# Kernel optimization log

Measured on AMD Instinct MI355X. Metric: run time of the kernel, lower is better.

## Reference

```python
import jax, jax.numpy as jnp
import numpy as np

N, D, E, K, L, NF, VOCAB = 100000, 128, 600000, 3, 3, 9, 100
BN_EPS = 1e-5
S = 0.05


def setup_inputs() -> dict:
    key = jax.random.key(0)
    ks = jax.random.split(key, 8)
    return {
        "x": jax.random.randint(ks[0], (N, NF), 0, VOCAB),
        "k_edges": jax.random.randint(ks[1], (K, 2, E), 0, N),
        "emb_tables": jax.random.normal(ks[2], (NF, VOCAB, D), jnp.float32) * S,
        "W1": jax.random.normal(ks[3], (L, D, 2 * D), jnp.float32) * S,
        "b1": jnp.zeros((L, 2 * D), jnp.float32),
        "g1": jnp.ones((L, 2 * D), jnp.float32),
        "be1": jnp.zeros((L, 2 * D), jnp.float32),
        "W2": jax.random.normal(ks[4], (L, 2 * D, D), jnp.float32) * S,
        "b2": jnp.zeros((L, D), jnp.float32),
        "eps": jnp.zeros((L,), jnp.float32),
        "alpha": jnp.zeros((L, K), jnp.float32),
        "bn_g": jnp.ones((L, D), jnp.float32),
        "bn_b": jnp.zeros((L, D), jnp.float32),
    }


def _bn(h, g, b):
    # training-mode BatchNorm1d over the node (batch) axis
    mu = h.mean(axis=0)
    var = h.var(axis=0)
    return (h - mu) * jax.lax.rsqrt(var + BN_EPS) * g + b


def _gin(h, src, dst, eps_l, W1_l, b1_l, g1_l, be1_l, W2_l, b2_l):
    # NodeGINConv (train_eps): mlp((1+eps)*x + sum_{j->i} x_j)
    agg = jax.ops.segment_sum(h[src], dst, num_segments=N)  # [N, D]
    z = (1.0 + eps_l) * h + agg
    z = jax.nn.relu(_bn(z @ W1_l + b1_l, g1_l, be1_l))  # [N, 2D]
    return z @ W2_l + b2_l  # [N, D]


def reference(x, k_edges, emb_tables, W1, b1, g1, be1, W2, b2, eps, alpha, bn_g, bn_b):
    # AtomEncoder: sum of per-feature embedding lookups -> [N, D]
    h = jnp.take_along_axis(
        emb_tables.transpose(1, 0, 2),  # [VOCAB, NF, D]
        x.T[..., None].transpose(1, 0, 2) * 0 + 0,  # placeholder avoided below
        axis=0,
    ) if False else emb_tables[jnp.arange(NF)[None, :], x].sum(axis=1)
    for l in range(L):
        # one shared wrapped GIN conv applied to each of the K relational edge sets
        msgs = jax.vmap(
            lambda e: _gin(h, e[0], e[1], eps[l], W1[l], b1[l], g1[l], be1[l], W2[l], b2[l])
        )(k_edges)  # [K, N, D]
        a = jax.nn.softmax(alpha[l])  # [K]
        h = jnp.einsum('knd,k->nd', msgs, a)
        h = jax.nn.relu(_bn(h, bn_g[l], bn_b[l]))  # dropout p=0 / eval -> identity
    return h
```

## Files before the change

### kernel.cpp

```cpp
#include <hip/hip_runtime.h>

#define NV     100000
#define DD     128
#define D2     256
#define EE     600000
#define KK     3
#define LL     3
#define NFEAT  9
#define VOCABS 100

#define NBKT   196
#define BCAP   8192

typedef __attribute__((ext_vector_type(8))) short short8;
typedef __attribute__((ext_vector_type(4))) float f32x4;
typedef __attribute__((ext_vector_type(2))) float f32x2;
typedef __attribute__((ext_vector_type(4))) unsigned int uint4v;

#define PA      0
#define PA2     8
#define PB2     136
#define PA1K(k) (264 + (k)*512)
#define PB1K(k) (264 + (k)*512 + 256)

#define ZS(k)  ((k)*512)
#define ZQ(k)  ((k)*512 + 256)
#define HSUM   1536
#define HSQ    1664

#define HB_OFF   ((size_t)0)
#define ZIN_OFF  ((size_t)25700000)
#define HNB_OFF  ((size_t)102500000)
#define O_BASE   ((size_t)128100000)

__device__ __forceinline__ unsigned short f2bf(float f) {
    union { float f; unsigned int u; } v; v.f = f;
    return (unsigned short)((v.u + 0x7FFFu + ((v.u >> 16) & 1u)) >> 16);
}
__device__ __forceinline__ float bf2f(unsigned short u) {
    union { unsigned int u; float f; } v; v.u = ((unsigned int)u) << 16;
    return v.f;
}
__device__ __forceinline__ f32x2 up2(unsigned int v) {
    union { unsigned int u[2]; f32x2 f; } w;
    w.u[0] = v << 16;
    w.u[1] = v & 0xFFFF0000u;
    return w.f;
}

__global__ void k_embed(const int* __restrict__ x, const float* __restrict__ emb,
                        unsigned short* __restrict__ hb) {
    int id = blockIdx.x*256 + threadIdx.x;
    int n = id >> 5, q = id & 31;
    if (n >= NV) {
        if (n < NV + 8) *(unsigned long long*)(hb + (size_t)n*DD + q*4) = 0ull;
        return;
    }
    const int* xr = x + n*NFEAT;
    f32x4 acc = {0.f,0.f,0.f,0.f};
    #pragma unroll
    for (int f = 0; f < NFEAT; ++f) {
        int idx = xr[f];
        acc += *(const f32x4*)(emb + ((size_t)(f*VOCABS + idx)*DD + q*4));
    }
    unsigned short pk[4];
    pk[0] = f2bf(acc[0]); pk[1] = f2bf(acc[1]); pk[2] = f2bf(acc[2]); pk[3] = f2bf(acc[3]);
    *(unsigned long long*)(hb + (size_t)n*DD + q*4) = *(unsigned long long*)pk;
}

__global__ void kA_bin(const int* __restrict__ ke, int* __restrict__ cursor,
                       uint2* __restrict__ pairs) {
    __shared__ int hist[NBKT], excl[NBKT], ofs[NBKT], gbase[NBKT];
    __shared__ int sc[256];
    __shared__ uint2 buf[4096];
    const int rel = blockIdx.y, t = threadIdx.x;
    const int e0 = blockIdx.x * 4096;
    const int cnt = min(4096, EE - e0);
    const int* srcA = ke + (size_t)(rel*2)*EE + e0;
    const int* dstA = ke + (size_t)(rel*2+1)*EE + e0;
    if (t < NBKT) hist[t] = 0;
    __syncthreads();
    for (int i = t; i < cnt; i += 256) atomicAdd(&hist[dstA[i] >> 9], 1);
    __syncthreads();
    const int hv = (t < NBKT) ? hist[t] : 0;
    sc[t] = hv;
    for (int off = 1; off < 256; off <<= 1) {
        __syncthreads();
        int v = (t >= off) ? sc[t-off] : 0;
        __syncthreads();
        sc[t] += v;
    }
    __syncthreads();
    if (t < NBKT) {
        excl[t] = sc[t] - hv;
        ofs[t]  = sc[t] - hv;
        if (hv > 0) gbase[t] = atomicAdd(&cursor[rel*NBKT + t], hv);
    }
    __syncthreads();
    for (int i = t; i < cnt; i += 256) {
        unsigned int s = (unsigned int)srcA[i], d = (unsigned int)dstA[i];
        int p = atomicAdd(&ofs[d >> 9], 1);
        uint2 u; u.x = s; u.y = d;
        buf[p] = u;
    }
    __syncthreads();
    for (int i = t; i < cnt; i += 256) {
        uint2 u = buf[i];
        int b = (int)(u.y >> 9);
        int pos = gbase[b] + (i - excl[b]);
        if (pos < BCAP) pairs[(size_t)(rel*NBKT + b)*BCAP + pos] = u;
    }
}

__global__ void kB_scan(const int* __restrict__ cursor, int* __restrict__ ebase) {
    __shared__ int sc[256];
    const int t = threadIdx.x;
    for (int rel = 0; rel < KK; ++rel) {
        int hv = (t < NBKT) ? min(cursor[rel*NBKT + t], BCAP) : 0;
        sc[t] = hv;
        for (int off = 1; off < 256; off <<= 1) {
            __syncthreads();
            int v = (t >= off) ? sc[t-off] : 0;
            __syncthreads();
            sc[t] += v;
        }
        __syncthreads();
        if (t < NBKT) ebase[rel*NBKT + t] = sc[t] - hv;
        __syncthreads();
    }
}

__global__ void kB_fill(const uint2* __restrict__ pairs, const int* __restrict__ cursor,
                        const int* __restrict__ ebase, int* __restrict__ rp,
                        int* __restrict__ col) {
    __shared__ int h2[512], excl[512], cur[512], sc[256];
    const int b = blockIdx.x, rel = blockIdx.y, t = threadIdx.x;
    const int lo = b * 512;
    const int cnt = min(cursor[rel*NBKT + b], BCAP);
    const int base = ebase[rel*NBKT + b];
    const uint2* P = pairs + (size_t)(rel*NBKT + b)*BCAP;
    h2[t] = 0; h2[t+256] = 0; cur[t] = 0; cur[t+256] = 0;
    __syncthreads();
    for (int i = t; i < cnt; i += 256) atomicAdd(&h2[(int)P[i].y - lo], 1);
    __syncthreads();
    const int a0 = h2[2*t], a1 = h2[2*t+1];
    sc[t] = a0 + a1;
    for (int off = 1; off < 256; off <<= 1) {
        __syncthreads();
        int v = (t >= off) ? sc[t-off] : 0;
        __syncthreads();
        sc[t] += v;
    }
    __syncthreads();
    const int e2 = sc[t] - (a0 + a1);
    excl[2*t] = e2; excl[2*t+1] = e2 + a0;
    __syncthreads();
    for (int tt = t; tt < 512; tt += 256) {
        int n = lo + tt;
        if (n <= NV) rp[(size_t)rel*(NV+1) + n] = base + excl[tt];
    }
    for (int i = t; i < cnt; i += 256) {
        uint2 u = P[i];
        int r = (int)u.y - lo;
        int p = atomicAdd(&cur[r], 1);
        col[(size_t)rel*EE + base + excl[r] + p] = (int)u.x;
    }
}

__global__ void k_prep(const float* __restrict__ W1, const float* __restrict__ W2,
                       const float* __restrict__ alpha, const int l,
                       unsigned short* __restrict__ w1f, unsigned short* __restrict__ w2f,
                       float* __restrict__ params) {
    int id = blockIdx.x*256 + threadIdx.x;
    if (id == 0) {
        float a0 = alpha[l*KK+0], a1 = alpha[l*KK+1], a2 = alpha[l*KK+2];
        float m = fmaxf(a0, fmaxf(a1, a2));
        float e0 = expf(a0-m), e1 = expf(a1-m), e2 = expf(a2-m);
        float inv = 1.f/(e0+e1+e2);
        params[PA+0] = e0*inv; params[PA+1] = e1*inv; params[PA+2] = e2*inv;
    }
    if (id < 4096) {
        int kt = id >> 10, nt = (id >> 6) & 15, lane = id & 63;
        int r = lane & 15, g = lane >> 4;
        const float* Wl = W1 + (size_t)l*DD*D2;
        #pragma unroll
        for (int e = 0; e < 8; ++e) {
            int kk = kt*32 + g*8 + e, c = nt*16 + r;
            w1f[(size_t)id*8 + e] = f2bf(Wl[(size_t)kk*D2 + c]);
        }
    } else if (id < 8192) {
        int id2 = id - 4096;
        int kt = id2 >> 9, nt = (id2 >> 6) & 7, lane = id2 & 63;
        int r = lane & 15, g = lane >> 4;
        const float* Wl = W2 + (size_t)l*D2*DD;
        #pragma unroll
        for (int e = 0; e < 8; ++e) {
            int kk = kt*32 + g*8 + e, c = nt*16 + r;
            w2f[(size_t)id2*8 + e] = f2bf(Wl[(size_t)kk*DD + c]);
        }
    }
}

__global__ void k_gather3(const unsigned short* __restrict__ hb, const int* __restrict__ rp,
                          const int* __restrict__ col, const float* __restrict__ epsp,
                          unsigned short* __restrict__ zin) {
    int gid = blockIdx.x*256 + threadIdx.x;
    int n0 = gid >> 6;
    if (n0 >= NV) return;
    const int n = __builtin_amdgcn_readfirstlane(n0);
    const int lane = threadIdx.x & 63;
    const int q = lane >> 4, r = lane & 15;
    const int r16 = r << 4;
    const char* hbase = (const char*)hb;
    const float epsv = 1.0f + epsp[0];
    const uint4v sv = *(const uint4v*)(hbase + (((unsigned)n << 8) + r16));
    int b0[KK], dg[KK], cv[KK];
    #pragma unroll
    for (int k = 0; k < KK; ++k) {
        int a = rp[k*(NV+1) + n];
        int b = rp[k*(NV+1) + n + 1];
        b0[k] = a; dg[k] = b - a;
        cv[k] = (lane < dg[k]) ? col[(size_t)k*EE + a + lane] : NV;
    }
    f32x2 acc[KK][4];
    #pragma unroll
    for (int k = 0; k < KK; ++k)
        #pragma unroll
        for (int c = 0; c < 4; ++c) acc[k][c] = (f32x2){0.f, 0.f};
    #pragma unroll
    for (int k = 0; k < KK; ++k) {
        const int dc = min(dg[k], 64);
        for (int base = 0; base < dc; base += 8) {
            int s0 = __shfl(cv[k], base + q);
            int s1 = __shfl(cv[k], base + q + 4);
            uint4v v0 = *(const uint4v*)(hbase + (((unsigned)s0 << 8) + r16));
            uint4v v1 = *(const uint4v*)(hbase + (((unsigned)s1 << 8) + r16));
            #pragma unroll
            for (int c = 0; c < 4; ++c) {
                acc[k][c] += up2(v0[c]);
                acc[k][c] += up2(v1[c]);
            }
        }
        for (int j = b0[k] + 64 + q; j < b0[k] + dg[k]; j += 4) {
            int s0 = col[(size_t)k*EE + j];
            uint4v v0 = *(const uint4v*)(hbase + (((unsigned)s0 << 8) + r16));
            #pragma unroll
            for (int c = 0; c < 4; ++c) acc[k][c] += up2(v0[c]);
        }
    }
    #pragma unroll
    for (int k = 0; k < KK; ++k) {
        #pragma unroll
        for (int c = 0; c < 4; ++c) {
            acc[k][c][0] += __shfl_xor(acc[k][c][0], 16);
            acc[k][c][1] += __shfl_xor(acc[k][c][1], 16);
            acc[k][c][0] += __shfl_xor(acc[k][c][0], 32);
            acc[k][c][1] += __shfl_xor(acc[k][c][1], 32);
        }
    }
    if (q == 0) {
        #pragma unroll
        for (int k = 0; k < KK; ++k) {
            uint4v pk;
            #pragma unroll
            for (int c = 0; c < 4; ++c) {
                f32x2 s2 = up2(sv[c]);
                float lo = acc[k][c][0] + epsv * s2[0];
                float hi = acc[k][c][1] + epsv * s2[1];
                unsigned int pko;
                asm("v_cvt_pk_bf16_f32 %0, %1, %2" : "=v"(pko) : "v"(lo), "v"(hi));
                pk[c] = pko;
            }
            *(uint4v*)((char*)zin + (size_t)k*NV*DD*2 + (((unsigned)n << 8) + r16)) = pk;
        }
    }
}

__launch_bounds__(256, 2)
__global__ void k_stats3(const unsigned short* __restrict__ zin,
                         const unsigned short* __restrict__ w1f,
                         float* __restrict__ stats) {
    __shared__ __align__(16) unsigned short bfr1[32768];
    __shared__ float scf[1024];
    const int t = threadIdx.x;
    const int krel = blockIdx.y;
    const unsigned short* zk = zin + (size_t)krel*NV*DD;
    float* zsum = stats + ZS(krel);
    float* zsq  = stats + ZQ(krel);
    for (int i = t; i < 4096; i += 256)
        *(uint4v*)(bfr1 + i*8) = *(const uint4v*)(w1f + i*8);
    const int lane = t & 63, w = t >> 6;
    const int r_ = lane & 15, g = lane >> 4;
    const int rt = w & 1, ch = w >> 1;
    __syncthreads();
    float ssum[8] = {0,0,0,0,0,0,0,0};
    float ssq[8]  = {0,0,0,0,0,0,0,0};
    for (int tile = blockIdx.x; tile < NV/32; tile += gridDim.x) {
        const int row0 = tile*32;
        short8 af[4];
        #pragma unroll
        for (int kt = 0; kt < 4; ++kt)
            af[kt] = *(const short8*)(zk + (size_t)(row0 + rt*16 + r_)*DD + kt*32 + g*8);
        #pragma unroll
        for (int ct = 0; ct < 8; ++ct) {
            const int ntg = ch*8 + ct;
            f32x4 c = {0.f,0.f,0.f,0.f};
            #pragma unroll
            for (int kt = 0; kt < 4; ++kt) {
                short8 b = *(const short8*)(bfr1 + ((size_t)((kt*16 + ntg)*64 + lane))*8);
                c = __builtin_amdgcn_mfma_f32_16x16x32_bf16(af[kt], b, c, 0, 0, 0);
            }
            float s = c[0]+c[1]+c[2]+c[3];
            float q = c[0]*c[0]+c[1]*c[1]+c[2]*c[2]+c[3]*c[3];
            s += __shfl_xor(s, 16); q += __shfl_xor(q, 16);
            s += __shfl_xor(s, 32); q += __shfl_xor(q, 32);
            ssum[ct] += s; ssq[ct] += q;
        }
    }
    if (g == 0) {
        #pragma unroll
        for (int ct = 0; ct < 8; ++ct) {
            const int colc = (ch*8 + ct)*16 + r_;
            scf[rt*256 + colc]       = ssum[ct];
            scf[512 + rt*256 + colc] = ssq[ct];
        }
    }
    __syncthreads();
    atomicAdd(zsum + t, scf[t]       + scf[256 + t]);
    atomicAdd(zsq  + t, scf[512 + t] + scf[768 + t]);
}

__global__ void k_bnprep3(float* __restrict__ stats,
                          const float* __restrict__ g1l, const float* __restrict__ be1l,
                          float* __restrict__ params) {
    int j = threadIdx.x;
    #pragma unroll
    for (int k = 0; k < KK; ++k) {
        float ak  = params[PA + k];
        float mu  = stats[ZS(k) + j] * (1.0f/NV);
        float var = stats[ZQ(k) + j] * (1.0f/NV) - mu*mu;
        float A = g1l[j] * rsqrtf(var + 1e-5f);
        params[PA1K(k) + j] = ak * A;
        params[PB1K(k) + j] = ak * (be1l[j] - mu*A);
        stats[ZS(k) + j] = 0.0f; stats[ZQ(k) + j] = 0.0f;
    }
}

#define GBODY2(YT) {                                                               \
    const int cur_ = tile;                                                         \
    short8 af[KK][4];                                                              \
    _Pragma("unroll")                                                              \
    for (int k = 0; k < KK; ++k) {                                                 \
        _Pragma("unroll")                                                          \
        for (int kt = 0; kt < 4; ++kt)                                             \
            af[k][kt] = *(const short8*)(zin + (size_t)k*NV*DD                     \
                          + (size_t)(cur_*32 + rt*16 + r_)*DD + kt*32 + g*8);      \
    }                                                                              \
    f32x4 y[2];                                                                    \
    y[0] = (f32x4){0.f,0.f,0.f,0.f};                                               \
    y[1] = (f32x4){0.f,0.f,0.f,0.f};                                               \
    _Pragma("unroll")                                                              \
    for (int k = 0; k < KK; ++k) {                                                 \
        _Pragma("unroll")                                                          \
        for (int ct = 0; ct < 2; ++ct) {                                           \
            const int ntg = ch*2 + ct;                                             \
            f32x4 c = {0.f,0.f,0.f,0.f};                                           \
            _Pragma("unroll")                                                      \
            for (int kt = 0; kt < 4; ++kt) {                                       \
                short8 b = *(const short8*)(bfr1 + ((size_t)((kt*16 + ntg)*64 + lane))*8); \
                c = __builtin_amdgcn_mfma_f32_16x16x32_bf16(af[k][kt], b, c, 0, 0, 0); \
            }                                                                      \
            _Pragma("unroll")                                                      \
            for (int reg = 0; reg < 4; ++reg)                                      \
                y[ct][reg] += fmaxf(pa1[k][ct]*c[reg] + pb1[k][ct], 0.0f);         \
        }                                                                          \
    }                                                                              \
    _Pragma("unroll")                                                              \
    for (int ct = 0; ct < 2; ++ct) {                                               \
        const int col2 = ((ch*2 + ct)*16 + r_)*2;                                  \
        _Pragma("unroll")                                                          \
        for (int reg = 0; reg < 4; ++reg) {                                        \
            const int row = rt*16 + g*4 + reg;                                     \
            *(unsigned short*)(YT + row*512 + (col2 ^ ((row & 15) << 4))) = f2bf(y[ct][reg]); \
        }                                                                          \
    }                                                                              \
    __syncthreads();                                                               \
    short8 ya[8];                                                                  \
    _Pragma("unroll")                                                              \
    for (int kt = 0; kt < 8; ++kt)                                                 \
        ya[kt] = *(const short8*)(YT + arow*512 + ((kt*64 + g*16) ^ ((arow & 15) << 4))); \
    f32x4 c2 = {0.f,0.f,0.f,0.f};                                                  \
    _Pragma("unroll")                                                              \
    for (int kt = 0; kt < 8; ++kt) {                                               \
        short8 b = *(const short8*)(bfr2 + ((size_t)((kt*8 + ch)*64 + lane))*8);   \
        c2 = __builtin_amdgcn_mfma_f32_16x16x32_bf16(ya[kt], b, c2, 0, 0, 0);      \
    }                                                                              \
    unsigned short* hp = hnb + (size_t)(cur_*32 + rt*16 + g*4)*DD + ch*16 + r_;    \
    float ps = 0.0f, pq = 0.0f;                                                    \
    _Pragma("unroll")                                                              \
    for (int reg = 0; reg < 4; ++reg) {                                            \
        float xv = c2[reg];                                                        \
        hp[(size_t)reg*DD] = f2bf(xv);                                             \
        ps += xv; pq += xv*xv;                                                     \
    }                                                                              \
    ps += __shfl_xor(ps, 16); pq += __shfl_xor(pq, 16);                            \
    ps += __shfl_xor(ps, 32); pq += __shfl_xor(pq, 32);                            \
    ssum0 += ps; ssq0 += pq;                                                       \
    tile += step;                                                                  \
}

__launch_bounds__(1024, 1)
__global__ void k_gemm2f(const unsigned short* __restrict__ zin,
                         const unsigned short* __restrict__ w1f,
                         const unsigned short* __restrict__ w2f,
                         const float* __restrict__ params,
                         unsigned short* __restrict__ hnb,
                         float* __restrict__ hsum, float* __restrict__ hsq) {
    __shared__ __align__(16) unsigned short bfr1[32768];
    __shared__ __align__(16) unsigned short bfr2[32768];
    __shared__ __align__(16) unsigned char ytA[16384];
    __shared__ __align__(16) unsigned char ytB[16384];
    const int t = threadIdx.x;
    for (int i = t; i < 4096; i += 1024)
        *(uint4v*)(bfr1 + i*8) = *(const uint4v*)(w1f + i*8);
    for (int i = t; i < 4096; i += 1024)
        *(uint4v*)(bfr2 + i*8) = *(const uint4v*)(w2f + i*8);
    const int lane = t & 63, w = t >> 6;
    const int r_ = lane & 15, g = lane >> 4;
    const int rt = w & 1, ch = w >> 1;
    const int arow = rt*16 + r_;
    float pa1[KK][2], pb1[KK][2];
    #pragma unroll
    for (int k = 0; k < KK; ++k) {
        #pragma unroll
        for (int ct = 0; ct < 2; ++ct) {
            const int colc = (ch*2 + ct)*16 + r_;
            pa1[k][ct] = params[PA1K(k) + colc];
            pb1[k][ct] = params[PB1K(k) + colc];
        }
    }
    __syncthreads();
    float ssum0 = 0.0f, ssq0 = 0.0f;
    const int NT = NV/32;
    const int step = gridDim.x;
    int tile = blockIdx.x;
    while (tile < NT) {
        GBODY2(ytA);
        if (tile >= NT) break;
        GBODY2(ytB);
    }
    __syncthreads();
    float* scf = (float*)ytA;
    if (g == 0) {
        scf[rt*128 + ch*16 + r_]       = ssum0;
        scf[256 + rt*128 + ch*16 + r_] = ssq0;
    }
    __syncthreads();
    if (t < 128) {
        atomicAdd(hsum + t, scf[t]       + scf[128 + t]);
        atomicAdd(hsq  + t, scf[256 + t] + scf[384 + t]);
    }
}

__global__ void k_bnprep2(float* __restrict__ hsum, float* __restrict__ hsq,
                          const float* __restrict__ bng, const float* __restrict__ bnb,
                          float* __restrict__ params) {
    int j = threadIdx.x;
    float mu  = hsum[j] * (1.0f/NV);
    float var = hsq[j]  * (1.0f/NV) - mu*mu;
    float A = bng[j] * rsqrtf(var + 1e-5f);
    params[PA2 + j] = A;
    params[PB2 + j] = bnb[j] - mu*A;
    hsum[j] = 0.0f; hsq[j] = 0.0f;
}

__global__ void k_bnapply_mid(const unsigned short* __restrict__ hnb,
                              const float* __restrict__ params,
                              unsigned short* __restrict__ hb) {
    int id = blockIdx.x*256 + threadIdx.x;
    const int col0 = (id & 15)*8;
    short8 v = *(const short8*)(hnb + (size_t)id*8);
    f32x4 A0 = *(const f32x4*)(params + PA2 + col0);
    f32x4 A1 = *(const f32x4*)(params + PA2 + col0 + 4);
    f32x4 B0 = *(const f32x4*)(params + PB2 + col0);
    f32x4 B1 = *(const f32x4*)(params + PB2 + col0 + 4);
    short8 o;
    #pragma unroll
    for (int j = 0; j < 4; ++j) {
        o[j]   = (short)f2bf(fmaxf(A0[j]*bf2f((unsigned short)v[j])   + B0[j], 0.0f));
        o[j+4] = (short)f2bf(fmaxf(A1[j]*bf2f((unsigned short)v[j+4]) + B1[j], 0.0f));
    }
    *(short8*)(hb + (size_t)id*8) = o;
}

__global__ void k_bnapply_fin(const unsigned short* __restrict__ hnb,
                              const float* __restrict__ params,
                              float* __restrict__ out) {
    int id = blockIdx.x*256 + threadIdx.x;
    const int col0 = (id & 15)*8;
    short8 v = *(const short8*)(hnb + (size_t)id*8);
    f32x4 A0 = *(const f32x4*)(params + PA2 + col0);
    f32x4 A1 = *(const f32x4*)(params + PA2 + col0 + 4);
    f32x4 B0 = *(const f32x4*)(params + PB2 + col0);
    f32x4 B1 = *(const f32x4*)(params + PB2 + col0 + 4);
    f32x4 o0, o1;
    #pragma unroll
    for (int j = 0; j < 4; ++j) {
        o0[j] = fmaxf(A0[j]*bf2f((unsigned short)v[j])   + B0[j], 0.0f);
        o1[j] = fmaxf(A1[j]*bf2f((unsigned short)v[j+4]) + B1[j], 0.0f);
    }
    *(f32x4*)(out + (size_t)id*8)     = o0;
    *(f32x4*)(out + (size_t)id*8 + 4) = o1;
}

extern "C" void kernel_launch(void* const* d_in, const int* in_sizes, int n_in,
                              void* d_out, int out_size, void* d_ws, size_t ws_size,
                              hipStream_t stream) {
    const int*   x     = (const int*)d_in[0];
    const int*   ke    = (const int*)d_in[1];
    const float* emb   = (const float*)d_in[2];
    const float* W1    = (const float*)d_in[3];
    const float* g1    = (const float*)d_in[5];
    const float* be1   = (const float*)d_in[6];
    const float* W2    = (const float*)d_in[7];
    const float* eps   = (const float*)d_in[9];
    const float* alpha = (const float*)d_in[10];
    const float* bng   = (const float*)d_in[11];
    const float* bnb   = (const float*)d_in[12];

    char* ws = (char*)d_ws;
    unsigned short* hb     = (unsigned short*)(ws + HB_OFF);
    unsigned short* zin    = (unsigned short*)(ws + ZIN_OFF);
    unsigned short* hnb    = (unsigned short*)(ws + HNB_OFF);
    size_t o = O_BASE;
    unsigned short* w1f    = (unsigned short*)(ws + o);          o += 65536;
    unsigned short* w2f    = (unsigned short*)(ws + o);          o += 65536;
    float*          stats  = (float*)(ws + o);                   o += 8192;
    float*          params = (float*)(ws + o);                   o += 8192;
    int*            rp     = (int*)(ws + o);                     o += 1200128;
    int*            col    = (int*)(ws + o);                     o += 7200000;
    int*            cur    = (int*)(ws + o);                     o += 4096;
    int*            ebase  = (int*)(ws + o);                     o += 4096;
    uint2*          pairs  = (uint2*)(ws + ZIN_OFF);

    k_embed<<<12501, 256, 0, stream>>>(x, emb, hb);

    hipMemsetAsync(cur, 0, KK*NBKT*sizeof(int), stream);
    hipMemsetAsync(stats, 0, 8192, stream);
    kA_bin<<<dim3(147, KK), 256, 0, stream>>>(ke, cur, pairs);
    kB_scan<<<1, 256, 0, stream>>>(cur, ebase);
    kB_fill<<<dim3(NBKT, KK), 256, 0, stream>>>(pairs, cur, ebase, rp, col);

    for (int l = 0; l < LL; ++l) {
        k_prep<<<32, 256, 0, stream>>>(W1, W2, alpha, l, w1f, w2f, params);
        k_gather3<<<25000, 256, 0, stream>>>(hb, rp, col, eps + l, zin);
        k_stats3<<<dim3(512, KK), 256, 0, stream>>>(zin, w1f, stats);
        k_bnprep3<<<1, 256, 0, stream>>>(stats, g1 + l*D2, be1 + l*D2, params);
        k_gemm2f<<<256, 1024, 0, stream>>>(zin, w1f, w2f, params, hnb,
                                           stats + HSUM, stats + HSQ);
        k_bnprep2<<<1, 128, 0, stream>>>(stats + HSUM, stats + HSQ,
                                         bng + l*DD, bnb + l*DD, params);
        if (l < LL-1) k_bnapply_mid<<<6250, 256, 0, stream>>>(hnb, params, hb);
        else          k_bnapply_fin<<<6250, 256, 0, stream>>>(hnb, params, (float*)d_out);
    }
}
```

Measured before the change: 803.0 us.

## Stage z tiles through LDS with register prefetch and hold W2 fragments in registers

The fused GEMM kernel now prefetches the next-next tile of the aggregated z input into registers and writes it into a swizzled, double-buffered LDS staging area, so global loads overlap with the current tile's MFMA work. Before, each wave did strided direct global loads into A fragments. The second-layer weights are now held per wave in registers instead of LDS, which frees LDS for the z staging buffers. The cost is higher register pressure and more LDS traffic, and the two-ahead prefetch bookkeeping adds complexity around the loop tail.

```diff
diff --git a/kernel.cpp b/kernel.cpp
--- a/kernel.cpp
+++ b/kernel.cpp
@@ -346,55 +346,66 @@
     }
 }
 
-#define GBODY2(YT) {                                                               \
+
+#define GLOAD(SA, SB, TT) {                                                        \
+    const char* p_ = (const char*)zin + (size_t)(TT)*8192;                         \
+    SA = *(const uint4v*)(p_ + gsrcA);                                             \
+    if (t < 512) SB = *(const uint4v*)(p_ + gsrcB);                                \
+}
+
+#define GITER(ZSRD, YTBUF, ZSWR, SWA, SWB, SLA, SLB) {                             \
     const int cur_ = tile;                                                         \
-    short8 af[KK][4];                                                              \
-    _Pragma("unroll")                                                              \
-    for (int k = 0; k < KK; ++k) {                                                 \
-        _Pragma("unroll")                                                          \
-        for (int kt = 0; kt < 4; ++kt)                                             \
-            af[k][kt] = *(const short8*)(zin + (size_t)k*NV*DD                     \
-                          + (size_t)(cur_*32 + rt*16 + r_)*DD + kt*32 + g*8);      \
-    }                                                                              \
+               \
     f32x4 y[2];                                                                    \
     y[0] = (f32x4){0.f,0.f,0.f,0.f};                                               \
     y[1] = (f32x4){0.f,0.f,0.f,0.f};                                               \
     _Pragma("unroll")                                                              \
     for (int k = 0; k < KK; ++k) {                                                 \
+        short8 af[4];                                                              \
+        _Pragma("unroll")                                                          \
+        for (int kt = 0; kt < 4; ++kt)                                             \
+            af[kt] = *(const short8*)(ZSRD + k*8192 + (rt*16 + r_)*256             \
+                         + ((((kt*4 + g) ^ r_) & 15) << 4));                       \
         _Pragma("unroll")                                                          \
         for (int ct = 0; ct < 2; ++ct) {                                           \
-            const int ntg = ch*2 + ct;                                             \
             f32x4 c = {0.f,0.f,0.f,0.f};                                           \
             _Pragma("unroll")                                                      \
             for (int kt = 0; kt < 4; ++kt) {                                       \
-                short8 b = *(const short8*)(bfr1 + ((size_t)((kt*16 + ntg)*64 + lane))*8); \
-                c = __builtin_amdgcn_mfma_f32_16x16x32_bf16(af[k][kt], b, c, 0, 0, 0); \
+                short8 b = *(const short8*)(bfr1 + ((size_t)((kt*16 + ch*2 + ct)*64 + lane))*8); \
+                c = __builtin_amdgcn_mfma_f32_16x16x32_bf16(af[kt], b, c, 0, 0, 0); \
             }                                                                      \
             _Pragma("unroll")                                                      \
             for (int reg = 0; reg < 4; ++reg)                                      \
                 y[ct][reg] += fmaxf(pa1[k][ct]*c[reg] + pb1[k][ct], 0.0f);         \
         }                                                                          \
     }                                                                              \
+                                                      \
     _Pragma("unroll")                                                              \
     for (int ct = 0; ct < 2; ++ct) {                                               \
         const int col2 = ((ch*2 + ct)*16 + r_)*2;                                  \
         _Pragma("unroll")                                                          \
         for (int reg = 0; reg < 4; ++reg) {                                        \
             const int row = rt*16 + g*4 + reg;                                     \
-            *(unsigned short*)(YT + row*512 + (col2 ^ ((row & 15) << 4))) = f2bf(y[ct][reg]); \
+            *(unsigned short*)(YTBUF + row*512 + (col2 ^ ((row & 15) << 4))) = f2bf(y[ct][reg]); \
         }                                                                          \
     }                                                                              \
+                    \
+    if (cur_ + step < NT) {                                                        \
+        *(uint4v*)(ZSWR + dstA) = SWA;                                             \
+        if (t < 512) *(uint4v*)(ZSWR + dstB) = SWB;                                \
+    }                                                                              \
     __syncthreads();                                                               \
+                                 \
+    if (cur_ + 2*step < NT) GLOAD(SLA, SLB, cur_ + 2*step);                        \
+                                            \
     short8 ya[8];                                                                  \
     _Pragma("unroll")                                                              \
     for (int kt = 0; kt < 8; ++kt)                                                 \
-        ya[kt] = *(const short8*)(YT + arow*512 + ((kt*64 + g*16) ^ ((arow & 15) << 4))); \
+        ya[kt] = *(const short8*)(YTBUF + arow*512 + ((kt*64 + g*16) ^ ((arow & 15) << 4))); \
     f32x4 c2 = {0.f,0.f,0.f,0.f};                                                  \
     _Pragma("unroll")                                                              \
-    for (int kt = 0; kt < 8; ++kt) {                                               \
-        short8 b = *(const short8*)(bfr2 + ((size_t)((kt*8 + ch)*64 + lane))*8);   \
-        c2 = __builtin_amdgcn_mfma_f32_16x16x32_bf16(ya[kt], b, c2, 0, 0, 0);      \
-    }                                                                              \
+    for (int kt = 0; kt < 8; ++kt)                                                 \
+        c2 = __builtin_amdgcn_mfma_f32_16x16x32_bf16(ya[kt], wb[kt], c2, 0, 0, 0); \
     unsigned short* hp = hnb + (size_t)(cur_*32 + rt*16 + g*4)*DD + ch*16 + r_;    \
     float ps = 0.0f, pq = 0.0f;                                                    \
     _Pragma("unroll")                                                              \
@@ -417,18 +428,21 @@
                          unsigned short* __restrict__ hnb,
                          float* __restrict__ hsum, float* __restrict__ hsq) {
     __shared__ __align__(16) unsigned short bfr1[32768];
-    __shared__ __align__(16) unsigned short bfr2[32768];
-    __shared__ __align__(16) unsigned char ytA[16384];
-    __shared__ __align__(16) unsigned char ytB[16384];
+    __shared__ __align__(16) unsigned char zs0[24576];
+    __shared__ __align__(16) unsigned char zs1[24576];
+    __shared__ __align__(16) unsigned char yt0[16384];
+    __shared__ __align__(16) unsigned char yt1[16384];
     const int t = threadIdx.x;
     for (int i = t; i < 4096; i += 1024)
         *(uint4v*)(bfr1 + i*8) = *(const uint4v*)(w1f + i*8);
-    for (int i = t; i < 4096; i += 1024)
-        *(uint4v*)(bfr2 + i*8) = *(const uint4v*)(w2f + i*8);
     const int lane = t & 63, w = t >> 6;
     const int r_ = lane & 15, g = lane >> 4;
     const int rt = w & 1, ch = w >> 1;
     const int arow = rt*16 + r_;
+    short8 wb[8];
+    #pragma unroll
+    for (int kt = 0; kt < 8; ++kt)
+        wb[kt] = *(const short8*)(w2f + ((size_t)((kt*8 + ch)*64 + lane))*8);
     float pa1[KK][2], pb1[KK][2];
     #pragma unroll
     for (int k = 0; k < KK; ++k) {
@@ -439,18 +453,30 @@
             pb1[k][ct] = params[PB1K(k) + colc];
         }
     }
-    __syncthreads();
-    float ssum0 = 0.0f, ssq0 = 0.0f;
+    const int kA = t >> 9, remA = t & 511, rowA = remA >> 4, cA = remA & 15;
+    const size_t gsrcA = (size_t)kA*((size_t)NV*256) + (size_t)rowA*256 + (size_t)cA*16;
+    const int dstA = kA*8192 + rowA*256 + (((cA ^ rowA) & 15) << 4);
+    const int rowB = (t & 511) >> 4, cB = t & 15;
+    const size_t gsrcB = (size_t)2*((size_t)NV*256) + (size_t)rowB*256 + (size_t)cB*16;
+    const int dstB = 2*8192 + rowB*256 + (((cB ^ rowB) & 15) << 4);
+
     const int NT = NV/32;
     const int step = gridDim.x;
     int tile = blockIdx.x;
+    uint4v s0A = {0,0,0,0}, s0B = {0,0,0,0}, s1A = {0,0,0,0}, s1B = {0,0,0,0};
+    GLOAD(s0A, s0B, tile);
+    *(uint4v*)(zs0 + dstA) = s0A;
+    if (t < 512) *(uint4v*)(zs0 + dstB) = s0B;
+    if (tile + step < NT) GLOAD(s1A, s1B, tile + step);
+    __syncthreads();
+    float ssum0 = 0.0f, ssq0 = 0.0f;
     while (tile < NT) {
-        GBODY2(ytA);
+        GITER(zs0, yt0, zs1, s1A, s1B, s0A, s0B);
         if (tile >= NT) break;
-        GBODY2(ytB);
-    }
-    __syncthreads();
-    float* scf = (float*)ytA;
+        GITER(zs1, yt1, zs0, s0A, s0B, s1A, s1B);
+    }
+    __syncthreads();
+    float* scf = (float*)yt0;
     if (g == 0) {
         scf[rt*128 + ch*16 + r_]       = ssum0;
         scf[256 + rt*128 + ch*16 + r_] = ssq0;
```

Measured after the change: 869.4 us. 8.3% more time.
